# Performance work log

Hardware: AMD Instinct MI355X
Metric: run time of the kernel (lower is better)

The kernel has to match this reference:

```python
import jax, jax.numpy as jnp
import numpy as np

D_MODEL = 1024
N_HEADS = 16
D_K = 64
BATCH = 2
SEQ = 2048
LN_EPS = 1e-5


def setup_inputs() -> dict:
    key = jax.random.key(0)
    ks = jax.random.split(key, 6)
    s = 1.0 / np.sqrt(D_MODEL)
    return {
        "h": jax.random.normal(ks[0], (BATCH, SEQ, D_MODEL), dtype=jnp.float32),
        "Wq": jax.random.normal(ks[1], (D_MODEL, D_MODEL), dtype=jnp.float32) * s,
        "bq": jnp.zeros((D_MODEL,), jnp.float32),
        "Wk": jax.random.normal(ks[2], (D_MODEL, D_MODEL), dtype=jnp.float32) * s,
        "bk": jnp.zeros((D_MODEL,), jnp.float32),
        "Wv": jax.random.normal(ks[3], (D_MODEL, D_MODEL), dtype=jnp.float32) * s,
        "bv": jnp.zeros((D_MODEL,), jnp.float32),
        "Wo": jax.random.normal(ks[4], (D_MODEL, D_MODEL), dtype=jnp.float32) * s,
        "bo": jnp.zeros((D_MODEL,), jnp.float32),
        "ln_w": jnp.ones((D_MODEL,), jnp.float32),
        "ln_b": jnp.zeros((D_MODEL,), jnp.float32),
    }


def _layernorm(x, w, b):
    mu = jnp.mean(x, axis=-1, keepdims=True)
    var = jnp.var(x, axis=-1, keepdims=True)
    return (x - mu) * jax.lax.rsqrt(var + LN_EPS) * w + b


def reference(h, Wq, bq, Wk, bk, Wv, bv, Wo, bo, ln_w, ln_b):
    b, s, _ = h.shape
    scale = 1.0 / np.sqrt(D_K)
    h_res = h
    hn = _layernorm(h, ln_w, ln_b)
    # Linear layers (torch convention: y = x @ W.T + b), split into heads
    q = (hn @ Wq.T + bq).reshape(b, s, N_HEADS, D_K)
    k = (hn @ Wk.T + bk).reshape(b, s, N_HEADS, D_K)
    v = (hn @ Wv.T + bv).reshape(b, s, N_HEADS, D_K)
    attn = jnp.einsum('bihd,bjhd->bhij', q, k) * scale  # [b, h, i, j]
    attn = jax.nn.softmax(attn, axis=-1)
    o = jnp.einsum('bhij,bjhd->bihd', attn, v).reshape(b, s, N_HEADS * D_K)
    out = o @ Wo.T + bo
    return out + h_res
```

## Files before the change

### kernel.cpp

```cpp
#include <hip/hip_runtime.h>
#include <cstdint>

#define D_MODEL 1024
#define N_HEADS 16
#define D_K     64
#define BATCH   2
#define SEQ     2048
#define TOKENS  (BATCH * SEQ)
#define LN_EPS  1e-5f
#define QSCALE  0.18033688011112042f

typedef __bf16 bf16x8 __attribute__((ext_vector_type(8)));
typedef float  floatx4  __attribute__((ext_vector_type(4)));
typedef float  floatx16 __attribute__((ext_vector_type(16)));

__device__ __forceinline__ unsigned short f2bf(float f) {
  union { float f; unsigned u; } v; v.f = f;
  unsigned r = v.u + 0x7fffu + ((v.u >> 16) & 1u);
  return (unsigned short)(r >> 16);
}
__device__ __forceinline__ unsigned pk2bf(float hi, float lo) {
  union { float f; unsigned u; } a, b;
  a.f = hi; b.f = lo;
  return __builtin_amdgcn_perm(a.u, b.u, 0x07060302u);
}

__device__ __forceinline__ void cp16(void* lds, const void* g) {
  __builtin_amdgcn_global_load_lds(
      (__attribute__((address_space(1))) void*)g,
      (__attribute__((address_space(3))) void*)lds, 16, 0, 0);
}

__global__ __launch_bounds__(256) void prep_kernel(
    const float* __restrict__ h, const float* __restrict__ w0,
    const float* __restrict__ w1, const float* __restrict__ w2,
    const float* __restrict__ w3, const float* __restrict__ lw,
    const float* __restrict__ lb, unsigned short* __restrict__ Wcat,
    unsigned short* __restrict__ hn) {
  if (blockIdx.x < 4096) {
    int wsel = blockIdx.x >> 10;
    const float* s = (wsel == 0) ? w0 : (wsel == 1) ? w1 : (wsel == 2) ? w2 : w3;
    unsigned short* d = Wcat + ((size_t)wsel << 20);
    int i = ((blockIdx.x & 1023) << 8) + threadIdx.x;
    float4 v = reinterpret_cast<const float4*>(s)[i];
    ushort4 o;
    o.x = f2bf(v.x); o.y = f2bf(v.y); o.z = f2bf(v.z); o.w = f2bf(v.w);
    reinterpret_cast<ushort4*>(d)[i] = o;
    return;
  }
  int row = blockIdx.x - 4096;
  const float* x = h + (size_t)row * D_MODEL;
  float4 v = reinterpret_cast<const float4*>(x)[threadIdx.x];
  float s  = v.x + v.y + v.z + v.w;
  float s2 = v.x * v.x + v.y * v.y + v.z * v.z + v.w * v.w;
  for (int m = 1; m < 64; m <<= 1) {
    s  += __shfl_xor(s, m);
    s2 += __shfl_xor(s2, m);
  }
  __shared__ float ls[4], ls2[4];
  int wave = threadIdx.x >> 6;
  if ((threadIdx.x & 63) == 0) { ls[wave] = s; ls2[wave] = s2; }
  __syncthreads();
  s  = ls[0] + ls[1] + ls[2] + ls[3];
  s2 = ls2[0] + ls2[1] + ls2[2] + ls2[3];
  float mu  = s * (1.0f / D_MODEL);
  float var = s2 * (1.0f / D_MODEL) - mu * mu;
  float rs  = rsqrtf(var + LN_EPS);
  float4 wv = reinterpret_cast<const float4*>(lw)[threadIdx.x];
  float4 bv = reinterpret_cast<const float4*>(lb)[threadIdx.x];
  ushort4 o;
  o.x = f2bf((v.x - mu) * rs * wv.x + bv.x);
  o.y = f2bf((v.y - mu) * rs * wv.y + bv.y);
  o.z = f2bf((v.z - mu) * rs * wv.z + bv.z);
  o.w = f2bf((v.w - mu) * rs * wv.w + bv.w);
  reinterpret_cast<ushort4*>(hn + (size_t)row * D_MODEL)[threadIdx.x] = o;
}

__global__ __launch_bounds__(256) void gemm_qkv_kernel(
    const unsigned short* __restrict__ A, const unsigned short* __restrict__ Wcat,
    const float* __restrict__ bq, const float* __restrict__ bk,
    const float* __restrict__ bv,
    unsigned short* __restrict__ QK, unsigned short* __restrict__ VtG) {
  __shared__ unsigned short As[128 * 64];
  __shared__ unsigned short Bs[128 * 64];

  const int tid  = threadIdx.x;
  const int w    = tid >> 6;
  const int lane = tid & 63;
  const int l15  = lane & 15;
  const int quad = lane >> 4;
  const int sw   = l15 & 7;
  const int wm = (w >> 1) * 64;
  const int wn = (w & 1) * 64;
  const int bm = blockIdx.y * 128;
  const int bn = blockIdx.x * 128;

  const int srow = tid >> 3;
  const int swzc = (((tid & 7) ^ (srow & 7)) * 8);
  const unsigned short* ga = A    + (size_t)(bm + srow) * 1024 + swzc;
  const unsigned short* gb = Wcat + (size_t)(bn + srow) * 1024 + swzc;
  unsigned short* asl = As + w * 512;
  unsigned short* bsl = Bs + w * 512;

  floatx4 acc[4][4];
  for (int i = 0; i < 4; ++i)
    for (int j = 0; j < 4; ++j) acc[i][j] = {0.f, 0.f, 0.f, 0.f};

  for (int k0 = 0; k0 < 1024; k0 += 64) {
#pragma unroll
    for (int i = 0; i < 4; ++i) cp16(asl + i * 2048, ga + (size_t)i * 32 * 1024 + k0);
#pragma unroll
    for (int i = 0; i < 4; ++i) cp16(bsl + i * 2048, gb + (size_t)i * 32 * 1024 + k0);
    __syncthreads();
#pragma unroll
    for (int kb = 0; kb < 2; ++kb) {
      bf16x8 af[4], bfr[4];
#pragma unroll
      for (int mi = 0; mi < 4; ++mi)
        af[mi] = *reinterpret_cast<const bf16x8*>(
            As + (wm + mi * 16 + l15) * 64 + (((kb * 4 + quad) ^ sw) * 8));
#pragma unroll
      for (int ni = 0; ni < 4; ++ni)
        bfr[ni] = *reinterpret_cast<const bf16x8*>(
            Bs + (wn + ni * 16 + l15) * 64 + (((kb * 4 + quad) ^ sw) * 8));
#pragma unroll
      for (int mi = 0; mi < 4; ++mi)
#pragma unroll
        for (int ni = 0; ni < 4; ++ni)
          acc[mi][ni] = __builtin_amdgcn_mfma_f32_16x16x32_bf16(af[mi], bfr[ni], acc[mi][ni], 0, 0, 0);
    }
    __syncthreads();
  }

  const int wsel = blockIdx.x >> 3;
  if (wsel == 0) {
#pragma unroll
    for (int mi = 0; mi < 4; ++mi)
#pragma unroll
      for (int ni = 0; ni < 4; ++ni) {
        int col = bn + wn + ni * 16 + l15;
        float bb = bq[col];
#pragma unroll
        for (int r = 0; r < 4; ++r) {
          int row = bm + wm + mi * 16 + quad * 4 + r;
          QK[(size_t)row * 2048 + col] = f2bf((acc[mi][ni][r] + bb) * QSCALE);
        }
      }
  } else if (wsel == 1) {
#pragma unroll
    for (int mi = 0; mi < 4; ++mi)
#pragma unroll
      for (int ni = 0; ni < 4; ++ni) {
        int col = bn + wn + ni * 16 + l15;
        float bb = bk[col - 1024];
#pragma unroll
        for (int r = 0; r < 4; ++r) {
          int row = bm + wm + mi * 16 + quad * 4 + r;
          QK[(size_t)row * 2048 + col] = f2bf(acc[mi][ni][r] + bb);
        }
      }
  } else {
#pragma unroll
    for (int mi = 0; mi < 4; ++mi)
#pragma unroll
      for (int ni = 0; ni < 4; ++ni) {
        int d = bn + wn + ni * 16 + l15 - 2048;
        float bb = bv[d];
        ushort4 o;
        o.x = f2bf(acc[mi][ni][0] + bb);
        o.y = f2bf(acc[mi][ni][1] + bb);
        o.z = f2bf(acc[mi][ni][2] + bb);
        o.w = f2bf(acc[mi][ni][3] + bb);
        int row0 = bm + wm + mi * 16 + quad * 4;
        *reinterpret_cast<ushort4*>(VtG + (size_t)d * 4096 + row0) = o;
      }
  }
}

__global__ __launch_bounds__(256) void gemm_out_kernel(
    const unsigned short* __restrict__ A, const unsigned short* __restrict__ Bt,
    const float* __restrict__ bo, const float* __restrict__ resid,
    float* __restrict__ out) {
  __shared__ unsigned short As[128 * 64];
  __shared__ unsigned short Bs[64 * 64];

  const int tid  = threadIdx.x;
  const int w    = tid >> 6;
  const int lane = tid & 63;
  const int l15  = lane & 15;
  const int quad = lane >> 4;
  const int sw   = l15 & 7;
  const int wm = (w >> 1) * 64;
  const int wn = (w & 1) * 32;
  const int bm = blockIdx.y * 128;
  const int bn = blockIdx.x * 64;

  const int srow = tid >> 3;
  const int swzc = (((tid & 7) ^ (srow & 7)) * 8);
  const unsigned short* ga = A  + (size_t)(bm + srow) * 1024 + swzc;
  const unsigned short* gb = Bt + (size_t)(bn + srow) * 1024 + swzc;
  unsigned short* asl = As + w * 512;
  unsigned short* bsl = Bs + w * 512;

  floatx4 acc[4][2];
  for (int i = 0; i < 4; ++i)
    for (int j = 0; j < 2; ++j) acc[i][j] = {0.f, 0.f, 0.f, 0.f};

  for (int k0 = 0; k0 < 1024; k0 += 64) {
#pragma unroll
    for (int i = 0; i < 4; ++i) cp16(asl + i * 2048, ga + (size_t)i * 32 * 1024 + k0);
#pragma unroll
    for (int i = 0; i < 2; ++i) cp16(bsl + i * 2048, gb + (size_t)i * 32 * 1024 + k0);
    __syncthreads();
#pragma unroll
    for (int kb = 0; kb < 2; ++kb) {
      bf16x8 af[4], bfr[2];
#pragma unroll
      for (int mi = 0; mi < 4; ++mi)
        af[mi] = *reinterpret_cast<const bf16x8*>(
            As + (wm + mi * 16 + l15) * 64 + (((kb * 4 + quad) ^ sw) * 8));
#pragma unroll
      for (int ni = 0; ni < 2; ++ni)
        bfr[ni] = *reinterpret_cast<const bf16x8*>(
            Bs + (wn + ni * 16 + l15) * 64 + (((kb * 4 + quad) ^ sw) * 8));
#pragma unroll
      for (int mi = 0; mi < 4; ++mi)
#pragma unroll
        for (int ni = 0; ni < 2; ++ni)
          acc[mi][ni] = __builtin_amdgcn_mfma_f32_16x16x32_bf16(af[mi], bfr[ni], acc[mi][ni], 0, 0, 0);
    }
    __syncthreads();
  }

#pragma unroll
  for (int mi = 0; mi < 4; ++mi)
#pragma unroll
    for (int ni = 0; ni < 2; ++ni) {
      int col = bn + wn + ni * 16 + l15;
      float bb = bo[col];
#pragma unroll
      for (int r = 0; r < 4; ++r) {
        int row = bm + wm + mi * 16 + quad * 4 + r;
        size_t idx = (size_t)row * 1024 + col;
        out[idx] = acc[mi][ni][r] + bb + resid[idx];
      }
    }
}

__global__ __launch_bounds__(512, 4) void attn_kernel(
    const unsigned short* __restrict__ QK, const unsigned short* __restrict__ VtG,
    unsigned short* __restrict__ O) {
  __shared__ unsigned short Ks[2][128 * 64];
  __shared__ unsigned short Vs[2][64 * 128];

  const int tid  = threadIdx.x;
  const int w    = tid >> 6;
  const int wq   = w & 3;
  const int kb0  = (w >> 2) * 2;
  const int lane = tid & 63;
  const int l31  = lane & 31;
  const int h    = lane >> 5;
  const int s7   = l31 & 7;

  const int hh = blockIdx.x, qt = blockIdx.y, bz = blockIdx.z;
  const int tq0  = bz * SEQ + qt * 128;
  const int hoff = hh * 64;

  bf16x8 qf[4];
  {
    const unsigned short* qp =
        QK + (size_t)(tq0 + wq * 32 + l31) * 2048 + hoff + h * 8;
#pragma unroll
    for (int kd = 0; kd < 4; ++kd)
      qf[kd] = *reinterpret_cast<const bf16x8*>(qp + kd * 16);
  }

  floatx16 oacc[2];
#pragma unroll
  for (int db = 0; db < 2; ++db)
#pragma unroll
    for (int r = 0; r < 16; ++r) oacc[db][r] = 0.f;
  float lsum = 0.f;

  const unsigned short* kg = QK + 1024 + hoff
      + (size_t)(bz * SEQ + (tid >> 3)) * 2048
      + (((tid & 7) ^ ((tid >> 3) & 7)) * 8);
  const unsigned short* vg = VtG
      + (size_t)(hoff + (tid >> 4)) * 4096 + bz * SEQ
      + (((tid & 15) ^ ((tid >> 4) & 7)) * 8);

  auto stage = [&](int kt, int b) {
    const unsigned short* kgi = kg + (size_t)(kt * 128) * 2048;
    const unsigned short* vgi = vg + kt * 128;
    unsigned short* ksl = Ks[b] + w * 512;
    unsigned short* vsl = Vs[b] + w * 512;
#pragma unroll
    for (int i = 0; i < 2; ++i) cp16(ksl + i * 4096, kgi + (size_t)(i * 64) * 2048);
#pragma unroll
    for (int i = 0; i < 2; ++i) cp16(vsl + i * 4096, vgi + (size_t)(i * 32) * 4096);
  };

  stage(0, 0);

  for (int kt = 0; kt < SEQ / 128; ++kt) {
    __syncthreads();
    if (kt + 1 < SEQ / 128) stage(kt + 1, (kt + 1) & 1);
    const unsigned short* Kb = Ks[kt & 1];
    const unsigned short* Vb = Vs[kt & 1];

    floatx16 ss[2];
#pragma unroll
    for (int kk = 0; kk < 2; ++kk)
#pragma unroll
      for (int r = 0; r < 16; ++r) ss[kk][r] = 0.f;
#pragma unroll
    for (int kk = 0; kk < 2; ++kk) {
      const int kb = kb0 + kk;
      const unsigned short* krow = Kb + (kb * 32 + l31) * 64;
#pragma unroll
      for (int kd = 0; kd < 4; ++kd) {
        bf16x8 kf = *reinterpret_cast<const bf16x8*>(
            krow + (((kd * 2 + h) ^ s7) * 8));
        ss[kk] = __builtin_amdgcn_mfma_f32_32x32x16_bf16(kf, qf[kd], ss[kk], 0, 0, 0);
      }
    }

#pragma unroll
    for (int kk = 0; kk < 2; ++kk) {
      const int kb = kb0 + kk;
      float e[16];
      float bs = 0.f;
#pragma unroll
      for (int r = 0; r < 16; ++r) {
        e[r] = __builtin_amdgcn_exp2f(ss[kk][r]);
        bs += e[r];
      }
      bs += __shfl_xor(bs, 32);
      lsum += bs;
      unsigned p[8];
#pragma unroll
      for (int i = 0; i < 8; ++i) p[i] = pk2bf(e[2 * i + 1], e[2 * i]);

#pragma unroll
      for (int sub = 0; sub < 2; ++sub) {
        unsigned pl0 = p[sub * 4 + 0], pl1 = p[sub * 4 + 1];
        unsigned ph0 = p[sub * 4 + 2], ph1 = p[sub * 4 + 3];
        unsigned rec0 = __shfl_xor((int)(h ? pl0 : ph0), 32);
        unsigned rec1 = __shfl_xor((int)(h ? pl1 : ph1), 32);
        union { unsigned u[4]; bf16x8 v; } pf;
        pf.u[0] = h ? rec0 : pl0;
        pf.u[1] = h ? rec1 : pl1;
        pf.u[2] = h ? ph0 : rec0;
        pf.u[3] = h ? ph1 : rec1;
#pragma unroll
        for (int db = 0; db < 2; ++db) {
          bf16x8 vf = *reinterpret_cast<const bf16x8*>(
              Vb + (db * 32 + l31) * 128 + (((kb * 4 + sub * 2 + h) ^ s7) * 8));
          oacc[db] = __builtin_amdgcn_mfma_f32_32x32x16_bf16(vf, pf.v, oacc[db], 0, 0, 0);
        }
      }
    }
  }

  __syncthreads();
  float* osc = (float*)&Ks[0][0];
  float* lsc = (float*)&Vs[0][0];
  if (w >= 4) {
    float* dst = osc + ((size_t)(wq * 64 + lane) * 32);
#pragma unroll
    for (int db = 0; db < 2; ++db)
#pragma unroll
      for (int r = 0; r < 16; ++r)
        dst[(db * 16 + r + lane) & 31] = oacc[db][r];
    lsc[wq * 64 + lane] = lsum;
  }
  __syncthreads();
  if (w < 4) {
    const float* src = osc + ((size_t)(wq * 64 + lane) * 32);
    lsum += lsc[wq * 64 + lane];
#pragma unroll
    for (int db = 0; db < 2; ++db)
#pragma unroll
      for (int r = 0; r < 16; ++r)
        oacc[db][r] += src[(db * 16 + r + lane) & 31];

    float inv = 1.0f / lsum;
    unsigned short* ob = O + (size_t)(tq0 + wq * 32 + l31) * 1024 + hoff;
#pragma unroll
    for (int db = 0; db < 2; ++db)
#pragma unroll
      for (int rg = 0; rg < 4; ++rg) {
        int d0 = db * 32 + rg * 8 + h * 4;
        uint2 ov;
        ov.x = pk2bf(oacc[db][rg * 4 + 1] * inv, oacc[db][rg * 4 + 0] * inv);
        ov.y = pk2bf(oacc[db][rg * 4 + 3] * inv, oacc[db][rg * 4 + 2] * inv);
        *reinterpret_cast<uint2*>(ob + d0) = ov;
      }
  }
}

extern "C" void kernel_launch(void* const* d_in, const int* in_sizes, int n_in,
                              void* d_out, int out_size, void* d_ws, size_t ws_size,
                              hipStream_t stream) {
  const float* h    = (const float*)d_in[0];
  const float* Wq   = (const float*)d_in[1];
  const float* bq   = (const float*)d_in[2];
  const float* Wk   = (const float*)d_in[3];
  const float* bk   = (const float*)d_in[4];
  const float* Wv   = (const float*)d_in[5];
  const float* bv   = (const float*)d_in[6];
  const float* Wo   = (const float*)d_in[7];
  const float* bo   = (const float*)d_in[8];
  const float* ln_w = (const float*)d_in[9];
  const float* ln_b = (const float*)d_in[10];
  float* out = (float*)d_out;

  unsigned short* ws = (unsigned short*)d_ws;
  const size_t WSZ = (size_t)1 << 20;
  unsigned short* Wcat = ws;
  unsigned short* hn   = Wcat + 4 * WSZ;
  unsigned short* QKb  = hn + (size_t)TOKENS * D_MODEL;
  unsigned short* VtG  = QKb + (size_t)TOKENS * 2048;
  unsigned short* Obuf = VtG + (size_t)D_MODEL * TOKENS;

  prep_kernel<<<8192, 256, 0, stream>>>(h, Wq, Wk, Wv, Wo, ln_w, ln_b, Wcat, hn);

  gemm_qkv_kernel<<<dim3(24, 32), 256, 0, stream>>>(hn, Wcat, bq, bk, bv, QKb, VtG);

  attn_kernel<<<dim3(N_HEADS, SEQ / 128, BATCH), 512, 0, stream>>>(QKb, VtG, Obuf);

  gemm_out_kernel<<<dim3(16, 32), 256, 0, stream>>>(Obuf, Wcat + 3 * WSZ, bo, h, out);
}
```

Before: 198.1 us.

## Enlarge QKV GEMM tiles to 256x192 with double-buffered LDS and block swizzle

Rewrites the QKV projection GEMM to use 512-thread blocks computing 256x192 output tiles (each wave a 64x96 subtile). LDS tiles are double-buffered so the next K slice loads while the current one is consumed, which drops one barrier per iteration. The grid becomes 256 blocks with a remapped block index for better L2 locality. The goal is more operand reuse per global load and overlap of memory with MFMA work, at the cost of more LDS (112 KB) and registers per block and fewer blocks than CUs, which can leave some units idle.

```diff
diff --git a/kernel.cpp b/kernel.cpp
--- a/kernel.cpp
+++ b/kernel.cpp
@@ -76,13 +76,13 @@
   reinterpret_cast<ushort4*>(hn + (size_t)row * D_MODEL)[threadIdx.x] = o;
 }
 
-__global__ __launch_bounds__(256) void gemm_qkv_kernel(
+__global__ __launch_bounds__(512, 2) void gemm_qkv_kernel(
     const unsigned short* __restrict__ A, const unsigned short* __restrict__ Wcat,
     const float* __restrict__ bq, const float* __restrict__ bk,
     const float* __restrict__ bv,
     unsigned short* __restrict__ QK, unsigned short* __restrict__ VtG) {
-  __shared__ unsigned short As[128 * 64];
-  __shared__ unsigned short Bs[128 * 64];
+  __shared__ unsigned short As[2][256 * 64];
+  __shared__ unsigned short Bs[2][192 * 64];
 
   const int tid  = threadIdx.x;
   const int w    = tid >> 6;
@@ -90,90 +90,88 @@
   const int l15  = lane & 15;
   const int quad = lane >> 4;
   const int sw   = l15 & 7;
-  const int wm = (w >> 1) * 64;
-  const int wn = (w & 1) * 64;
-  const int bm = blockIdx.y * 128;
-  const int bn = blockIdx.x * 128;
+  const int wrow = (w >> 1) * 64;
+  const int wcol = (w & 1) * 96;
+
+  const int flat  = blockIdx.x + (blockIdx.y << 4);
+  const int swzid = ((flat & 7) << 5) + (flat >> 3);
+  const int bm = (swzid >> 4) * 256;
+  const int bn = (swzid & 15) * 192;
 
   const int srow = tid >> 3;
   const int swzc = (((tid & 7) ^ (srow & 7)) * 8);
   const unsigned short* ga = A    + (size_t)(bm + srow) * 1024 + swzc;
   const unsigned short* gb = Wcat + (size_t)(bn + srow) * 1024 + swzc;
-  unsigned short* asl = As + w * 512;
-  unsigned short* bsl = Bs + w * 512;
-
-  floatx4 acc[4][4];
+
+  floatx4 acc[4][6];
+#pragma unroll
   for (int i = 0; i < 4; ++i)
-    for (int j = 0; j < 4; ++j) acc[i][j] = {0.f, 0.f, 0.f, 0.f};
-
-  for (int k0 = 0; k0 < 1024; k0 += 64) {
-#pragma unroll
-    for (int i = 0; i < 4; ++i) cp16(asl + i * 2048, ga + (size_t)i * 32 * 1024 + k0);
-#pragma unroll
-    for (int i = 0; i < 4; ++i) cp16(bsl + i * 2048, gb + (size_t)i * 32 * 1024 + k0);
+#pragma unroll
+    for (int j = 0; j < 6; ++j) acc[i][j] = {0.f, 0.f, 0.f, 0.f};
+
+  auto stage = [&](int k0, int b) {
+    unsigned short* asl = &As[b][0] + w * 512;
+    unsigned short* bsl = &Bs[b][0] + w * 512;
+#pragma unroll
+    for (int i = 0; i < 4; ++i) cp16(asl + i * 4096, ga + (size_t)i * 64 * 1024 + k0);
+#pragma unroll
+    for (int i = 0; i < 3; ++i) cp16(bsl + i * 4096, gb + (size_t)i * 64 * 1024 + k0);
+  };
+
+  stage(0, 0);
+
+  for (int t = 0; t < 16; ++t) {
     __syncthreads();
+    if (t + 1 < 16) stage((t + 1) * 64, (t + 1) & 1);
+    const unsigned short* Ab = &As[t & 1][0];
+    const unsigned short* Bb = &Bs[t & 1][0];
 #pragma unroll
     for (int kb = 0; kb < 2; ++kb) {
-      bf16x8 af[4], bfr[4];
+      bf16x8 af[4], bfr[6];
 #pragma unroll
       for (int mi = 0; mi < 4; ++mi)
         af[mi] = *reinterpret_cast<const bf16x8*>(
-            As + (wm + mi * 16 + l15) * 64 + (((kb * 4 + quad) ^ sw) * 8));
-#pragma unroll
-      for (int ni = 0; ni < 4; ++ni)
+            Ab + (wrow + mi * 16 + l15) * 64 + (((kb * 4 + quad) ^ sw) * 8));
+#pragma unroll
+      for (int ni = 0; ni < 6; ++ni)
         bfr[ni] = *reinterpret_cast<const bf16x8*>(
-            Bs + (wn + ni * 16 + l15) * 64 + (((kb * 4 + quad) ^ sw) * 8));
+            Bb + (wcol + ni * 16 + l15) * 64 + (((kb * 4 + quad) ^ sw) * 8));
 #pragma unroll
       for (int mi = 0; mi < 4; ++mi)
 #pragma unroll
-        for (int ni = 0; ni < 4; ++ni)
+        for (int ni = 0; ni < 6; ++ni)
           acc[mi][ni] = __builtin_amdgcn_mfma_f32_16x16x32_bf16(af[mi], bfr[ni], acc[mi][ni], 0, 0, 0);
     }
-    __syncthreads();
-  }
-
-  const int wsel = blockIdx.x >> 3;
-  if (wsel == 0) {
-#pragma unroll
-    for (int mi = 0; mi < 4; ++mi)
-#pragma unroll
-      for (int ni = 0; ni < 4; ++ni) {
-        int col = bn + wn + ni * 16 + l15;
+  }
+
+#pragma unroll
+  for (int mi = 0; mi < 4; ++mi) {
+    const int row0 = bm + wrow + mi * 16 + quad * 4;
+#pragma unroll
+    for (int ni = 0; ni < 6; ++ni) {
+      const int cb  = bn + wcol + ni * 16;
+      const int col = cb + l15;
+      if (cb < 1024) {
         float bb = bq[col];
 #pragma unroll
-        for (int r = 0; r < 4; ++r) {
-          int row = bm + wm + mi * 16 + quad * 4 + r;
-          QK[(size_t)row * 2048 + col] = f2bf((acc[mi][ni][r] + bb) * QSCALE);
-        }
-      }
-  } else if (wsel == 1) {
-#pragma unroll
-    for (int mi = 0; mi < 4; ++mi)
-#pragma unroll
-      for (int ni = 0; ni < 4; ++ni) {
-        int col = bn + wn + ni * 16 + l15;
+        for (int r = 0; r < 4; ++r)
+          QK[(size_t)(row0 + r) * 2048 + col] = f2bf((acc[mi][ni][r] + bb) * QSCALE);
+      } else if (cb < 2048) {
         float bb = bk[col - 1024];
 #pragma unroll
-        for (int r = 0; r < 4; ++r) {
-          int row = bm + wm + mi * 16 + quad * 4 + r;
-          QK[(size_t)row * 2048 + col] = f2bf(acc[mi][ni][r] + bb);
-        }
-      }
-  } else {
-#pragma unroll
-    for (int mi = 0; mi < 4; ++mi)
-#pragma unroll
-      for (int ni = 0; ni < 4; ++ni) {
-        int d = bn + wn + ni * 16 + l15 - 2048;
+        for (int r = 0; r < 4; ++r)
+          QK[(size_t)(row0 + r) * 2048 + col] = f2bf(acc[mi][ni][r] + bb);
+      } else {
+        int d = col - 2048;
         float bb = bv[d];
         ushort4 o;
         o.x = f2bf(acc[mi][ni][0] + bb);
         o.y = f2bf(acc[mi][ni][1] + bb);
         o.z = f2bf(acc[mi][ni][2] + bb);
         o.w = f2bf(acc[mi][ni][3] + bb);
-        int row0 = bm + wm + mi * 16 + quad * 4;
         *reinterpret_cast<ushort4*>(VtG + (size_t)d * 4096 + row0) = o;
       }
+    }
   }
 }
 
@@ -425,7 +423,7 @@
 
   prep_kernel<<<8192, 256, 0, stream>>>(h, Wq, Wk, Wv, Wo, ln_w, ln_b, Wcat, hn);
 
-  gemm_qkv_kernel<<<dim3(24, 32), 256, 0, stream>>>(hn, Wcat, bq, bk, bv, QKb, VtG);
+  gemm_qkv_kernel<<<dim3(16, 16), 512, 0, stream>>>(hn, Wcat, bq, bk, bv, QKb, VtG);
 
   attn_kernel<<<dim3(N_HEADS, SEQ / 128, BATCH), 512, 0, stream>>>(QKb, VtG, Obuf);
 
```

Measured after the change: 200.1 us. No clear change (+1.0%).
